# Optimization experiments

Hardware: AMD Instinct MI355X
Metric: run time of the kernel (lower is better)

The kernel has to match this reference:

```python
import jax, jax.numpy as jnp
import numpy as np

B, DIM_IN, DIM_OUT = 8192, 2048, 512


def setup_inputs() -> dict:
    key = jax.random.key(0)
    k1, k2, k3, k4, k5 = jax.random.split(key, 5)
    s_in = 1.0 / np.sqrt(DIM_IN)
    return {
        "x": jax.random.normal(k1, (B, DIM_IN), dtype=jnp.float32),
        "W_hazard": jax.random.normal(k2, (DIM_OUT, DIM_IN), dtype=jnp.float32) * s_in,
        "b_hazard": jax.random.normal(k3, (DIM_OUT,), dtype=jnp.float32) * s_in,
        "W_base": jax.random.normal(k4, (1, DIM_IN), dtype=jnp.float32) * s_in,
        "b_base": jax.random.normal(k5, (1,), dtype=jnp.float32) * s_in,
    }


def reference(x, W_hazard, b_hazard, W_base, b_base):
    # hazards = ReLU(x @ W_h^T + b_h)  -> [B, T]
    hazards = jax.nn.relu(jnp.einsum("bd,td->bt", x, W_hazard) + b_hazard)
    # Triangular-mask expand+sum is exactly an inclusive prefix sum along T:
    # cum_prob[b, j] = sum_{i <= j} hazards[b, i] + base_hazard[b]
    cum_hazards = jnp.cumsum(hazards, axis=1)
    base_hazard = jnp.einsum("bd,od->bo", x, W_base) + b_base  # [B, 1]
    return cum_hazards + base_hazard
```

## Files before the change

### kernel.cpp

```cpp
#include <hip/hip_runtime.h>
#include <hip/hip_bf16.h>


typedef __attribute__((ext_vector_type(8))) short  short8;
typedef __attribute__((ext_vector_type(4))) short  short4v;
typedef __attribute__((ext_vector_type(4))) float  float4v;
typedef __attribute__((ext_vector_type(4))) float  f32x4;

#define DIN  2048
#define DOUT 512
#define NROW 8192
#define BM   32
#define NPH  (DIN / 64)
#define CHP  8
#define NCH  (NPH / CHP)

static __device__ __forceinline__ unsigned short f2bf(float f) {
  union { float f; unsigned int u; } v; v.f = f;
  unsigned int u = v.u;
  unsigned int r = (u + 0x7FFFu + ((u >> 16) & 1u)) >> 16;
  return (unsigned short)r;
}

static __device__ __forceinline__ void barrier_nd() {
  asm volatile("s_waitcnt lgkmcnt(0)" ::: "memory");
  __builtin_amdgcn_s_barrier();
}

__global__ __launch_bounds__(256) void k_pack(const float* __restrict__ W,
                                              unsigned short* __restrict__ Wp) {
  int t    = blockIdx.x * 256 + threadIdx.x;
  int lane = t & 63;
  int frag = t >> 6;
  int nt   = frag >> 6, ktp = frag & 63;
  int n = nt * 16 + (lane & 15);
  int k = ktp * 32 + (lane >> 4) * 8;
  const float* src = W + (size_t)n * DIN + k;
  float4v a = *(const float4v*)src;
  float4v b = *(const float4v*)(src + 4);
  unsigned short o[8] = { f2bf(a.x), f2bf(a.y), f2bf(a.z), f2bf(a.w),
                          f2bf(b.x), f2bf(b.y), f2bf(b.z), f2bf(b.w) };
  *(short8*)(Wp + (size_t)t * 8) = *(const short8*)o;
}

__global__ __launch_bounds__(1024, 4) void k_main(
    const float* __restrict__ x, const unsigned short* __restrict__ Wp,
    const float* __restrict__ b_h, const float* __restrict__ w_base,
    const float* __restrict__ b_base, float* __restrict__ out) {
  __shared__ unsigned short Achk[2][CHP * BM * 64];
  __shared__ float WbL[DIN];
  __shared__ float stripT[BM][16];
  __shared__ float baseL[BM];

  const int tid  = threadIdx.x;
  const int lane = tid & 63;
  const int w    = tid >> 6;
  const int q    = lane >> 4;
  const int lm   = lane & 15;
  const int m0   = blockIdx.x * BM;

  const int sr  = tid >> 5;
  const int cs  = (tid & 31) * 16;
  const int sph = cs >> 6;
  const int sg0 = (cs & 63) >> 3;
  const int offW0 = sph * 2048 + sr * 64 + (((sg0)     ^ (sr & 7)) << 3);
  const int offW1 = sph * 2048 + sr * 64 + (((sg0 + 1) ^ (sr & 7)) << 3);

  for (int i = tid; i < DIN; i += 1024) WbL[i] = w_base[i];

  f32x4 acc[2][2];
  const f32x4 z4 = {0.f, 0.f, 0.f, 0.f};
#pragma unroll
  for (int mi = 0; mi < 2; ++mi)
#pragma unroll
    for (int ni = 0; ni < 2; ++ni) acc[mi][ni] = z4;

  float4v st[4];
  float   basePart = 0.f;

  auto stage_load = [&](int c) {
    const float* p = x + (size_t)(m0 + sr) * DIN + c * (CHP * 64) + cs;
#pragma unroll
    for (int i = 0; i < 4; ++i) st[i] = *(const float4v*)(p + i * 4);
  };
  auto stage_write = [&](unsigned short* buf, int c) {
    unsigned short t16[16];
#pragma unroll
    for (int i = 0; i < 4; ++i) {
      t16[i * 4 + 0] = f2bf(st[i].x); t16[i * 4 + 1] = f2bf(st[i].y);
      t16[i * 4 + 2] = f2bf(st[i].z); t16[i * 4 + 3] = f2bf(st[i].w);
      const float4v wb = *(const float4v*)&WbL[c * (CHP * 64) + cs + i * 4];
      basePart += st[i].x * wb.x + st[i].y * wb.y + st[i].z * wb.z + st[i].w * wb.w;
    }
    *(short8*)&buf[offW0] = *(const short8*)&t16[0];
    *(short8*)&buf[offW1] = *(const short8*)&t16[8];
  };
  auto compute = [&](const unsigned short* buf, int c) {
#pragma unroll
    for (int ph = 0; ph < CHP; ++ph) {
      const int pk = c * CHP + ph;
      short8 bf[2][2];
#pragma unroll
      for (int ni = 0; ni < 2; ++ni)
#pragma unroll
        for (int h = 0; h < 2; ++h) {
          int frag = (w * 2 + ni) * 64 + pk * 2 + h;
          bf[ni][h] = *(const short8*)(Wp + ((size_t)frag << 9) + lane * 8);
        }
#pragma unroll
      for (int h = 0; h < 2; ++h) {
        short8 xf[2];
#pragma unroll
        for (int mi = 0; mi < 2; ++mi) {
          int r = mi * 16 + lm;
          int g = q + 4 * h;
          xf[mi] = *(const short8*)&buf[ph * 2048 + r * 64 + ((g ^ (r & 7)) << 3)];
        }
#pragma unroll
        for (int mi = 0; mi < 2; ++mi)
#pragma unroll
          for (int ni = 0; ni < 2; ++ni)
            acc[mi][ni] = __builtin_amdgcn_mfma_f32_16x16x32_bf16(
                bf[ni][h], xf[mi], acc[mi][ni], 0, 0, 0);
      }
    }
  };

  stage_load(0);
  barrier_nd();
  stage_write(Achk[0], 0);
  barrier_nd();

  for (int c = 0; c < NCH; ++c) {
    if (c + 1 < NCH) stage_load(c + 1);
    compute(Achk[c & 1], c);
    if (c + 1 < NCH) stage_write(Achk[(c + 1) & 1], c + 1);
    barrier_nd();
  }

  {
    float s = basePart;
    s += __shfl_xor(s, 1);  s += __shfl_xor(s, 2);
    s += __shfl_xor(s, 4);  s += __shfl_xor(s, 8);
    s += __shfl_xor(s, 16);
    if ((tid & 31) == 0) baseL[sr] = s + b_base[0];
  }

  float runp[2][2][4];
  float Eq[2][2];
  float niPre[2][2];
  float Tst[2];
#pragma unroll
  for (int mi = 0; mi < 2; ++mi) {
    float run = 0.f;
#pragma unroll
    for (int ni = 0; ni < 2; ++ni) {
      float4v b4 = *(const float4v*)(b_h + w * 32 + ni * 16 + q * 4);
      f32x4 v = acc[mi][ni];
      float h0 = fmaxf(v.x + b4.x, 0.f);
      float h1 = fmaxf(v.y + b4.y, 0.f);
      float h2 = fmaxf(v.z + b4.z, 0.f);
      float h3 = fmaxf(v.w + b4.w, 0.f);
      runp[mi][ni][0] = h0;
      runp[mi][ni][1] = h0 + h1;
      runp[mi][ni][2] = h0 + h1 + h2;
      runp[mi][ni][3] = h0 + h1 + h2 + h3;
      float S = runp[mi][ni][3];
      float u1 = __shfl_up(S, 16);
      float u2 = __shfl_up(S, 32);
      float u3 = __shfl_up(S, 48);
      Eq[mi][ni] = (q >= 1 ? u1 : 0.f) + (q >= 2 ? u2 : 0.f) + (q >= 3 ? u3 : 0.f);
      float G = S + __shfl_xor(S, 16);
      G += __shfl_xor(G, 32);
      niPre[mi][ni] = run;
      run += G;
    }
    Tst[mi] = run;
  }
  if (q == 0) {
#pragma unroll
    for (int mi = 0; mi < 2; ++mi) stripT[mi * 16 + lm][w] = Tst[mi];
  }
  barrier_nd();

#pragma unroll
  for (int mi = 0; mi < 2; ++mi) {
    const int row = mi * 16 + lm;
    float c = baseL[row];
#pragma unroll
    for (int j4 = 0; j4 < 4; ++j4) {
      float4v s = *(const float4v*)&stripT[row][j4 * 4];
      c += (w > j4 * 4 + 0 ? s.x : 0.f) + (w > j4 * 4 + 1 ? s.y : 0.f) +
           (w > j4 * 4 + 2 ? s.z : 0.f) + (w > j4 * 4 + 3 ? s.w : 0.f);
    }
#pragma unroll
    for (int ni = 0; ni < 2; ++ni) {
      float base = c + niPre[mi][ni] + Eq[mi][ni];
      float4v o = { runp[mi][ni][0] + base, runp[mi][ni][1] + base,
                    runp[mi][ni][2] + base, runp[mi][ni][3] + base };
      *(float4v*)(out + (size_t)(m0 + row) * DOUT + w * 32 + ni * 16 + q * 4) = o;
    }
  }
}

extern "C" void kernel_launch(void* const* d_in, const int* in_sizes, int n_in,
                              void* d_out, int out_size, void* d_ws, size_t ws_size,
                              hipStream_t stream) {
  const float* x   = (const float*)d_in[0];
  const float* Wh  = (const float*)d_in[1];
  const float* bh  = (const float*)d_in[2];
  const float* Wb0 = (const float*)d_in[3];
  const float* bb  = (const float*)d_in[4];
  float* out = (float*)d_out;

  unsigned short* Wp = (unsigned short*)d_ws;

  k_pack<<<dim3((DOUT * DIN) / (256 * 8)), dim3(256), 0, stream>>>(Wh, Wp);
  k_main<<<dim3(NROW / BM), dim3(1024), 0, stream>>>(x, Wp, bh, Wb0, bb, out);
}
```

Baseline: 50.41 us.

## Stream packed W tiles into LDS via global_load_lds double buffering per phase

Replaces the direct per-wave global loads of packed bf16 W fragments with asynchronous global-to-LDS DMA (global_load_lds) into a double-buffered LDS tile, advanced one 64-wide K phase at a time. The x staging is also cut from 8-phase chunks to one phase per iteration with float2 loads, and the occupancy hint in launch_bounds is dropped. The goal is to overlap W fetches with MFMA work and cut register pressure. In exchange it adds a barrier and a full vmcnt(0) wait on every one of 32 phases. Each wave also reads back only fragments it DMA'd itself, so the LDS hop adds latency without any sharing, and the larger LDS footprint may lower occupancy.

```diff
diff --git a/kernel.cpp b/kernel.cpp
--- a/kernel.cpp
+++ b/kernel.cpp
@@ -3,23 +3,28 @@
 
 
 typedef __attribute__((ext_vector_type(8))) short  short8;
-typedef __attribute__((ext_vector_type(4))) short  short4v;
 typedef __attribute__((ext_vector_type(4))) float  float4v;
 typedef __attribute__((ext_vector_type(4))) float  f32x4;
+typedef __attribute__((ext_vector_type(2))) float  float2v;
 
 #define DIN  2048
 #define DOUT 512
 #define NROW 8192
 #define BM   32
 #define NPH  (DIN / 64)
-#define CHP  8
-#define NCH  (NPH / CHP)
 
 static __device__ __forceinline__ unsigned short f2bf(float f) {
   union { float f; unsigned int u; } v; v.f = f;
   unsigned int u = v.u;
   unsigned int r = (u + 0x7FFFu + ((u >> 16) & 1u)) >> 16;
   return (unsigned short)r;
+}
+
+static __device__ __forceinline__ void dma16(const unsigned short* g,
+                                             unsigned short* l) {
+  __builtin_amdgcn_global_load_lds(
+      (const __attribute__((address_space(1))) unsigned int*)g,
+      (__attribute__((address_space(3))) unsigned int*)l, 16, 0, 0);
 }
 
 static __device__ __forceinline__ void barrier_nd() {
@@ -43,11 +48,12 @@
   *(short8*)(Wp + (size_t)t * 8) = *(const short8*)o;
 }
 
-__global__ __launch_bounds__(1024, 4) void k_main(
+__global__ __launch_bounds__(1024) void k_main(
     const float* __restrict__ x, const unsigned short* __restrict__ Wp,
     const float* __restrict__ b_h, const float* __restrict__ w_base,
     const float* __restrict__ b_base, float* __restrict__ out) {
-  __shared__ unsigned short Achk[2][CHP * BM * 64];
+  __shared__ unsigned short Bb[2][32 * 1024];
+  __shared__ unsigned short Aa[2][BM * 64];
   __shared__ float WbL[DIN];
   __shared__ float stripT[BM][16];
   __shared__ float baseL[BM];
@@ -60,13 +66,11 @@
   const int m0   = blockIdx.x * BM;
 
   const int sr  = tid >> 5;
-  const int cs  = (tid & 31) * 16;
-  const int sph = cs >> 6;
-  const int sg0 = (cs & 63) >> 3;
-  const int offW0 = sph * 2048 + sr * 64 + (((sg0)     ^ (sr & 7)) << 3);
-  const int offW1 = sph * 2048 + sr * 64 + (((sg0 + 1) ^ (sr & 7)) << 3);
-
-  for (int i = tid; i < DIN; i += 1024) WbL[i] = w_base[i];
+  const int c2  = (tid & 31) * 2;
+  const int sgA = c2 >> 3;
+  const int aOff = sr * 64 + ((sgA ^ (sr & 7)) << 3) + (c2 & 7);
+
+  ((float2v*)WbL)[tid] = ((const float2v*)w_base)[tid];
 
   f32x4 acc[2][2];
   const f32x4 z4 = {0.f, 0.f, 0.f, 0.f};
@@ -75,66 +79,71 @@
 #pragma unroll
     for (int ni = 0; ni < 2; ++ni) acc[mi][ni] = z4;
 
-  float4v st[4];
+  float2v aNext;
   float   basePart = 0.f;
 
-  auto stage_load = [&](int c) {
-    const float* p = x + (size_t)(m0 + sr) * DIN + c * (CHP * 64) + cs;
-#pragma unroll
-    for (int i = 0; i < 4; ++i) st[i] = *(const float4v*)(p + i * 4);
-  };
-  auto stage_write = [&](unsigned short* buf, int c) {
-    unsigned short t16[16];
-#pragma unroll
-    for (int i = 0; i < 4; ++i) {
-      t16[i * 4 + 0] = f2bf(st[i].x); t16[i * 4 + 1] = f2bf(st[i].y);
-      t16[i * 4 + 2] = f2bf(st[i].z); t16[i * 4 + 3] = f2bf(st[i].w);
-      const float4v wb = *(const float4v*)&WbL[c * (CHP * 64) + cs + i * 4];
-      basePart += st[i].x * wb.x + st[i].y * wb.y + st[i].z * wb.z + st[i].w * wb.w;
-    }
-    *(short8*)&buf[offW0] = *(const short8*)&t16[0];
-    *(short8*)&buf[offW1] = *(const short8*)&t16[8];
-  };
-  auto compute = [&](const unsigned short* buf, int c) {
-#pragma unroll
-    for (int ph = 0; ph < CHP; ++ph) {
-      const int pk = c * CHP + ph;
-      short8 bf[2][2];
-#pragma unroll
-      for (int ni = 0; ni < 2; ++ni)
-#pragma unroll
-        for (int h = 0; h < 2; ++h) {
-          int frag = (w * 2 + ni) * 64 + pk * 2 + h;
-          bf[ni][h] = *(const short8*)(Wp + ((size_t)frag << 9) + lane * 8);
-        }
+  auto dmaB = [&](int p, int buf) {
+#pragma unroll
+    for (int j = 0; j < 4; ++j) {
+      const int f = w * 4 + j;
+      const int fg = (f >> 1) * 64 + p * 2 + (f & 1);
+      dma16(Wp + (size_t)fg * 512 + lane * 8, &Bb[buf][f * 512]);
+    }
+  };
+  auto loadA = [&](int p) {
+    aNext = *(const float2v*)(x + (size_t)(m0 + sr) * DIN + p * 64 + c2);
+  };
+  auto stageA = [&](int p, unsigned short* Ad) {
+    unsigned int pk = ((unsigned int)f2bf(aNext.x)) |
+                      (((unsigned int)f2bf(aNext.y)) << 16);
+    *(unsigned int*)&Ad[aOff] = pk;
+    float2v wb = *(const float2v*)&WbL[p * 64 + c2];
+    basePart += aNext.x * wb.x + aNext.y * wb.y;
+  };
+  auto compute = [&](const unsigned short* Bc, const unsigned short* Ac) {
+    short8 bfr[2][2], xf[2][2];
+#pragma unroll
+    for (int h = 0; h < 2; ++h)
+#pragma unroll
+      for (int mi = 0; mi < 2; ++mi) {
+        int r = mi * 16 + lm;
+        int g = q + 4 * h;
+        xf[h][mi] = *(const short8*)&Ac[r * 64 + ((g ^ (r & 7)) << 3)];
+      }
+#pragma unroll
+    for (int ni = 0; ni < 2; ++ni)
 #pragma unroll
       for (int h = 0; h < 2; ++h) {
-        short8 xf[2];
-#pragma unroll
-        for (int mi = 0; mi < 2; ++mi) {
-          int r = mi * 16 + lm;
-          int g = q + 4 * h;
-          xf[mi] = *(const short8*)&buf[ph * 2048 + r * 64 + ((g ^ (r & 7)) << 3)];
-        }
-#pragma unroll
-        for (int mi = 0; mi < 2; ++mi)
-#pragma unroll
-          for (int ni = 0; ni < 2; ++ni)
-            acc[mi][ni] = __builtin_amdgcn_mfma_f32_16x16x32_bf16(
-                bf[ni][h], xf[mi], acc[mi][ni], 0, 0, 0);
+        int f = 4 * w + 2 * ni + h;
+        bfr[ni][h] = *(const short8*)&Bb[0][0];
+        bfr[ni][h] = *(const short8*)&Bc[f * 512 + lane * 8];
       }
-    }
-  };
-
-  stage_load(0);
+#pragma unroll
+    for (int h = 0; h < 2; ++h)
+#pragma unroll
+      for (int mi = 0; mi < 2; ++mi)
+#pragma unroll
+        for (int ni = 0; ni < 2; ++ni)
+          acc[mi][ni] = __builtin_amdgcn_mfma_f32_16x16x32_bf16(
+              bfr[ni][h], xf[h][mi], acc[mi][ni], 0, 0, 0);
+  };
+
+  dmaB(0, 0);
+  loadA(0);
   barrier_nd();
-  stage_write(Achk[0], 0);
+  stageA(0, Aa[0]);
+  asm volatile("s_waitcnt vmcnt(0)" ::: "memory");
   barrier_nd();
 
-  for (int c = 0; c < NCH; ++c) {
-    if (c + 1 < NCH) stage_load(c + 1);
-    compute(Achk[c & 1], c);
-    if (c + 1 < NCH) stage_write(Achk[(c + 1) & 1], c + 1);
+  for (int p = 0; p < NPH; ++p) {
+    const int cur = p & 1, nxt = cur ^ 1;
+    if (p + 1 < NPH) {
+      dmaB(p + 1, nxt);
+      loadA(p + 1);
+    }
+    compute(Bb[cur], Aa[cur]);
+    if (p + 1 < NPH) stageA(p + 1, Aa[nxt]);
+    asm volatile("s_waitcnt vmcnt(0)" ::: "memory");
     barrier_nd();
   }
 
```

Result: slower. 58.53 us (+16.1%).
